# Kernel tuning notes

Measured on AMD Instinct MI355X. Metric: run time of the kernel, lower is better.

The kernel has to match this reference:

```python
import jax, jax.numpy as jnp
import numpy as np

SPATIAL_SHAPES = ((80, 80), (40, 40), (20, 20))  # strides 8/16/32 on 640x640
NUM_HEADS = 8
N_POINTS = 4
D_MODEL = 256
OFFSET_SCALE = 0.5
N_LEVELS = len(SPATIAL_SHAPES)
TOTAL_P = N_LEVELS * N_POINTS


def setup_inputs() -> dict:
    key = jax.random.key(0)
    ks = jax.random.split(key, 11)
    B, Q = 32, 300
    S = sum(h * w for h, w in SPATIAL_SHAPES)  # 8400
    d = D_MODEL
    s = 0.02
    return {
        "hidden_states": jax.random.normal(ks[0], (B, Q, d), jnp.float32),
        "encoder_hidden_states": jax.random.normal(ks[1], (B, S, d), jnp.float32),
        "reference_points": jax.random.uniform(ks[2], (B, Q, 1, 4), jnp.float32, 0.1, 0.9),
        "W_off": jax.random.normal(ks[3], (d, NUM_HEADS * TOTAL_P * 2), jnp.float32) * s,
        "b_off": jax.random.normal(ks[4], (NUM_HEADS * TOTAL_P * 2,), jnp.float32) * s,
        "W_attn": jax.random.normal(ks[5], (d, NUM_HEADS * TOTAL_P), jnp.float32) * s,
        "b_attn": jax.random.normal(ks[6], (NUM_HEADS * TOTAL_P,), jnp.float32) * s,
        "W_val": jax.random.normal(ks[7], (d, d), jnp.float32) * s,
        "b_val": jax.random.normal(ks[8], (d,), jnp.float32) * s,
        "W_out": jax.random.normal(ks[9], (d, d), jnp.float32) * s,
        "b_out": jax.random.normal(ks[10], (d,), jnp.float32) * s,
    }


def _bilinear_sample(img, grid):
    # img: (N, H, W, C); grid: (N, Q, P, 2), normalized coords in [-1, 1]
    # torch grid_sample(mode='bilinear', padding_mode='zeros', align_corners=False)
    N, Hh, Ww, C = img.shape
    gx = (grid[..., 0] + 1.0) * (Ww * 0.5) - 0.5
    gy = (grid[..., 1] + 1.0) * (Hh * 0.5) - 0.5
    x0 = jnp.floor(gx)
    y0 = jnp.floor(gy)
    wx1 = gx - x0
    wx0 = 1.0 - wx1
    wy1 = gy - y0
    wy0 = 1.0 - wy1
    n_idx = jnp.arange(N)[:, None, None]

    def tap(ix, iy, w):
        valid = (ix >= 0) & (ix < Ww) & (iy >= 0) & (iy < Hh)
        ixc = jnp.clip(ix, 0, Ww - 1).astype(jnp.int32)
        iyc = jnp.clip(iy, 0, Hh - 1).astype(jnp.int32)
        v = img[n_idx, iyc, ixc]  # (N, Q, P, C)
        return v * (w * valid.astype(w.dtype))[..., None]

    return (tap(x0, y0, wx0 * wy0) + tap(x0 + 1.0, y0, wx1 * wy0)
            + tap(x0, y0 + 1.0, wx0 * wy1) + tap(x0 + 1.0, y0 + 1.0, wx1 * wy1))


def reference(hidden_states, encoder_hidden_states, reference_points,
              W_off, b_off, W_attn, b_attn, W_val, b_val, W_out, b_out):
    B, Q, d = hidden_states.shape
    S = encoder_hidden_states.shape[1]
    H = NUM_HEADS
    C = d // H

    value = (encoder_hidden_states @ W_val + b_val).reshape(B, S, H, C)
    offs = (hidden_states @ W_off + b_off).reshape(B, Q, H, TOTAL_P, 2)
    attn = jax.nn.softmax((hidden_states @ W_attn + b_attn).reshape(B, Q, H, TOTAL_P), axis=-1)

    # 4-d reference points branch (boxes): loc = ref_xy + off * (1/P) * ref_wh * offset_scale
    n_points_scale = jnp.full((TOTAL_P, 1), 1.0 / N_POINTS, hidden_states.dtype)
    loc = (reference_points[:, :, None, :, :2]
           + offs * n_points_scale * reference_points[:, :, None, :, 2:] * OFFSET_SCALE)
    grids = 2.0 * loc - 1.0  # method='default'
    grids = grids.transpose(0, 2, 1, 3, 4).reshape(B * H, Q, TOTAL_P, 2)

    value_bh = value.transpose(0, 2, 1, 3).reshape(B * H, S, C)

    samples = []
    start = 0
    p0 = 0
    for (h, w) in SPATIAL_SHAPES:
        v_l = value_bh[:, start:start + h * w].reshape(B * H, h, w, C)
        g_l = grids[:, :, p0:p0 + N_POINTS]
        samples.append(_bilinear_sample(v_l, g_l))
        start += h * w
        p0 += N_POINTS
    sampled = jnp.concatenate(samples, axis=2)  # (B*H, Q, TOTAL_P, C)

    attn_bh = attn.transpose(0, 2, 1, 3).reshape(B * H, Q, TOTAL_P)
    out = jnp.einsum("nqpc,nqp->nqc", sampled, attn_bh)  # (B*H, Q, C)
    out = out.reshape(B, H, Q, C).transpose(0, 2, 1, 3).reshape(B, Q, H * C)
    return out @ W_out + b_out
```

## Files before the change

### kernel.cpp

```cpp
#include <hip/hip_runtime.h>
#include <hip/hip_fp16.h>

#define DEVI __device__ __forceinline__

typedef _Float16 f16x8 __attribute__((ext_vector_type(8)));
typedef float f32x4 __attribute__((ext_vector_type(4)));

static DEVI unsigned short f2h_u(float f) {
    _Float16 h = (_Float16)f;
    return __builtin_bit_cast(unsigned short, h);
}
static DEVI float h2f_u(unsigned short u) {
    return (float)__builtin_bit_cast(_Float16, u);
}
static DEVI unsigned pk2(float a, float b) {
    return (unsigned)f2h_u(a) | ((unsigned)f2h_u(b) << 16);
}


__global__ __launch_bounds__(256) void prep_weights(
    const float* __restrict__ W_val, const float* __restrict__ W_off,
    const float* __restrict__ W_attn, const float* __restrict__ W_out,
    const float* __restrict__ b_off, const float* __restrict__ b_attn,
    unsigned short* __restrict__ Wvt, unsigned short* __restrict__ Wct,
    unsigned short* __restrict__ Wot, float* __restrict__ cbias)
{
    int idx = blockIdx.x * 256 + threadIdx.x;
    if (idx < 65536) {
        int n = idx >> 8, k = idx & 255;
        Wvt[idx] = f2h_u(W_val[k * 256 + n]);
    } else if (idx < 65536 + 73728) {
        int j = idx - 65536;
        int n = j >> 8, k = j & 255;
        Wct[j] = f2h_u(n < 192 ? W_off[k * 192 + n] : W_attn[k * 96 + (n - 192)]);
    } else if (idx < 204800) {
        int j = idx - 139264;
        int n = j >> 8, k = j & 255;
        Wot[j] = f2h_u(W_out[k * 256 + n]);
    } else if (idx < 205088) {
        int j = idx - 204800;
        cbias[j] = (j < 192) ? b_off[j] : b_attn[j - 192];
    }
}

template<int BN, bool OUT_F16>
__global__ __launch_bounds__(256) void gemm_f16(
    const float* __restrict__ A, const unsigned short* __restrict__ Wt,
    const float* __restrict__ bias, void* __restrict__ outp, int ldo)
{
    constexpr int NI  = BN / 16;
    constexpr int LDA = 40;
    constexpr int LDB = 40;
    constexpr int LDC = BN + 4;
    constexpr int SM1 = 64 * LDA * 2 + BN * LDB * 2;
    constexpr int SM2 = 64 * LDC * 4;
    constexpr int SMEM = SM1 > SM2 ? SM1 : SM2;
    __shared__ __align__(16) char smem[SMEM];
    unsigned short* As = (unsigned short*)smem;
    unsigned short* Bs = (unsigned short*)(smem + 64 * LDA * 2);
    float* Cs = (float*)smem;

    const int tid  = threadIdx.x;
    const int wave = tid >> 6;
    const int lane = tid & 63;
    const int l15  = lane & 15;
    const int qd   = lane >> 4;
    const int m0   = blockIdx.y * 64;
    const int n0   = blockIdx.x * BN;

    f32x4 acc[NI];
#pragma unroll
    for (int i = 0; i < NI; i++) acc[i] = (f32x4){0.f, 0.f, 0.f, 0.f};

#pragma unroll
    for (int kt = 0; kt < 8; kt++) {
#pragma unroll
        for (int i = 0; i < 2; i++) {
            int f = tid + i * 256;
            int row = f >> 3, c4 = f & 7;
            const float4 v = *(const float4*)(A + (size_t)(m0 + row) * 256 + kt * 32 + c4 * 4);
            uint2 p;
            p.x = pk2(v.x, v.y);
            p.y = pk2(v.z, v.w);
            *(uint2*)&As[row * LDA + c4 * 4] = p;
        }
        for (int f = tid; f < BN * 4; f += 256) {
            int row = f >> 2, ch = f & 3;
            uint4 v = *(const uint4*)(Wt + (size_t)(n0 + row) * 256 + kt * 32 + ch * 8);
            *(uint4*)&Bs[row * LDB + ch * 8] = v;
        }
        __syncthreads();
        f16x8 af = *(const f16x8*)&As[(wave * 16 + l15) * LDA + qd * 8];
#pragma unroll
        for (int ni = 0; ni < NI; ni++) {
            f16x8 fb = *(const f16x8*)&Bs[(ni * 16 + l15) * LDB + qd * 8];
            acc[ni] = __builtin_amdgcn_mfma_f32_16x16x32_f16(af, fb, acc[ni], 0, 0, 0);
        }
        __syncthreads();
    }

#pragma unroll
    for (int ni = 0; ni < NI; ni++) {
#pragma unroll
        for (int r = 0; r < 4; r++) {
            Cs[(wave * 16 + qd * 4 + r) * LDC + ni * 16 + l15] = acc[ni][r];
        }
    }
    __syncthreads();
    for (int f = tid; f < 64 * (BN / 4); f += 256) {
        int row = f / (BN / 4), c4 = f % (BN / 4);
        float4 v = *(const float4*)&Cs[row * LDC + c4 * 4];
        const float4 bb = *(const float4*)(bias + n0 + c4 * 4);
        v.x += bb.x; v.y += bb.y; v.z += bb.z; v.w += bb.w;
        if (OUT_F16) {
            uint2 p;
            p.x = pk2(v.x, v.y);
            p.y = pk2(v.z, v.w);
            *(uint2*)((unsigned short*)outp + (size_t)(m0 + row) * ldo + n0 + c4 * 4) = p;
        } else {
            *(float4*)((float*)outp + (size_t)(m0 + row) * ldo + n0 + c4 * 4) = v;
        }
    }
}

__global__ __launch_bounds__(256) void sample_attn(
    const float* __restrict__ P, const float* __restrict__ refp,
    const unsigned short* __restrict__ val, float* __restrict__ out_attn)
{
    __shared__ float sLog[8][12];
    __shared__ float sLoc[8][12][3];
    const int row = blockIdx.x;
    const int b = row / 300;
    const int tid = threadIdx.x;

    const float4 r4 = *(const float4*)(refp + (size_t)row * 4);

    int h = 0, p = 0;
    float offx = 0.f, offy = 0.f, logit = 0.f;
    if (tid < 96) {
        h = tid / 12;
        p = tid - h * 12;
        const float* Pr = P + (size_t)row * 288;
        offx  = Pr[h * 24 + p * 2];
        offy  = Pr[h * 24 + p * 2 + 1];
        logit = Pr[192 + h * 12 + p];
        sLog[h][p] = logit;
    }
    __syncthreads();
    if (tid < 96) {
        float m = -1e30f;
#pragma unroll
        for (int j = 0; j < 12; j++) m = fmaxf(m, sLog[h][j]);
        float s = 0.f;
#pragma unroll
        for (int j = 0; j < 12; j++) s += expf(sLog[h][j] - m);
        float w = expf(logit - m) / s;
        sLoc[h][p][0] = r4.x + offx * 0.125f * r4.z;
        sLoc[h][p][1] = r4.y + offy * 0.125f * r4.w;
        sLoc[h][p][2] = w;
    }
    __syncthreads();

    const int hh = tid >> 5, c = tid & 31;
    const unsigned short* vb = val + (size_t)b * 8400 * 256 + hh * 32 + c;
    float acc = 0.f;
#pragma unroll
    for (int p2 = 0; p2 < 12; p2++) {
        const int lvl  = p2 >> 2;
        const int W    = (lvl == 0) ? 80 : ((lvl == 1) ? 40 : 20);
        const int Hh   = W;
        const int loff = (lvl == 0) ? 0 : ((lvl == 1) ? 6400 : 8000);
        const float lx = sLoc[hh][p2][0];
        const float ly = sLoc[hh][p2][1];
        const float w  = sLoc[hh][p2][2];
        const float px = lx * (float)W - 0.5f;
        const float py = ly * (float)Hh - 0.5f;
        const float x0f = floorf(px), y0f = floorf(py);
        const float fx = px - x0f, fy = py - y0f;
        const int x0 = (int)x0f, y0 = (int)y0f;
        const int x1 = x0 + 1, y1 = y0 + 1;
        const float w00 = (1.f - fx) * (1.f - fy);
        const float w10 = fx * (1.f - fy);
        const float w01 = (1.f - fx) * fy;
        const float w11 = fx * fy;
        const bool vx0 = (x0 >= 0) && (x0 < W);
        const bool vx1 = (x1 >= 0) && (x1 < W);
        const bool vy0 = (y0 >= 0) && (y0 < Hh);
        const bool vy1 = (y1 >= 0) && (y1 < Hh);
        const int x0c = min(max(x0, 0), W - 1), x1c = min(max(x1, 0), W - 1);
        const int y0c = min(max(y0, 0), Hh - 1), y1c = min(max(y1, 0), Hh - 1);
        const float v00 = h2f_u(vb[(size_t)(loff + y0c * W + x0c) * 256]);
        const float v10 = h2f_u(vb[(size_t)(loff + y0c * W + x1c) * 256]);
        const float v01 = h2f_u(vb[(size_t)(loff + y1c * W + x0c) * 256]);
        const float v11 = h2f_u(vb[(size_t)(loff + y1c * W + x1c) * 256]);
        float sv = 0.f;
        sv += (vx0 && vy0) ? w00 * v00 : 0.f;
        sv += (vx1 && vy0) ? w10 * v10 : 0.f;
        sv += (vx0 && vy1) ? w01 * v01 : 0.f;
        sv += (vx1 && vy1) ? w11 * v11 : 0.f;
        acc += w * sv;
    }
    out_attn[(size_t)row * 256 + tid] = acc;
}

extern "C" void kernel_launch(void* const* d_in, const int* in_sizes, int n_in,
                              void* d_out, int out_size, void* d_ws, size_t ws_size,
                              hipStream_t stream)
{
    const float* hs     = (const float*)d_in[0];
    const float* enc    = (const float*)d_in[1];
    const float* refp   = (const float*)d_in[2];
    const float* W_off  = (const float*)d_in[3];
    const float* b_off  = (const float*)d_in[4];
    const float* W_attn = (const float*)d_in[5];
    const float* b_attn = (const float*)d_in[6];
    const float* W_val  = (const float*)d_in[7];
    const float* b_val  = (const float*)d_in[8];
    const float* W_out  = (const float*)d_in[9];
    const float* b_out  = (const float*)d_in[10];
    float* outp = (float*)d_out;

    char* ws = (char*)d_ws;
    unsigned short* val = (unsigned short*)ws;
    float* P            = (float*)(ws + 137625600);
    float* oattn        = (float*)(ws + 148684800);
    unsigned short* Wvt = (unsigned short*)(ws + 158515200);
    unsigned short* Wct = (unsigned short*)(ws + 158646272);
    unsigned short* Wot = (unsigned short*)(ws + 158793728);
    float* cbias        = (float*)(ws + 158924800);

    prep_weights<<<802, 256, 0, stream>>>(W_val, W_off, W_attn, W_out,
                                          b_off, b_attn, Wvt, Wct, Wot, cbias);
    gemm_f16<144, false><<<dim3(2, 150), 256, 0, stream>>>(hs, Wct, cbias, P, 288);
    gemm_f16<128, true ><<<dim3(2, 4200), 256, 0, stream>>>(enc, Wvt, b_val, val, 256);
    sample_attn<<<9600, 256, 0, stream>>>(P, refp, val, oattn);
    gemm_f16<128, false><<<dim3(2, 150), 256, 0, stream>>>(oattn, Wot, b_out, outp, 256);
}
```

Measured before the change: 543.0 us.

## Prefetch GEMM tiles into registers and write f16 epilogue directly

The GEMM main loop now loads the next k-tile of A and W into registers while the current tile is being multiplied, so global loads overlap with MFMA work. The f16-output path adds the bias and converts to half before staging, which halves the shared-memory footprint and lets stores be 16-byte wide. The small projection GEMMs also use narrower N tiles (96 and 64) so they launch more blocks. The risks are higher register pressure from the prefetch buffers and more redundant A loads across the extra N blocks.

```diff
diff --git a/kernel.cpp b/kernel.cpp
--- a/kernel.cpp
+++ b/kernel.cpp
@@ -49,16 +49,18 @@
     const float* __restrict__ bias, void* __restrict__ outp, int ldo)
 {
     constexpr int NI  = BN / 16;
+    constexpr int NB  = (BN * 4 + 255) / 256;
+    constexpr bool BEXACT = (BN * 4 % 256) == 0;
     constexpr int LDA = 40;
     constexpr int LDB = 40;
     constexpr int LDC = BN + 4;
+    constexpr int LDH = BN + 8;
     constexpr int SM1 = 64 * LDA * 2 + BN * LDB * 2;
-    constexpr int SM2 = 64 * LDC * 4;
+    constexpr int SM2 = OUT_F16 ? (64 * LDH * 2) : (64 * LDC * 4);
     constexpr int SMEM = SM1 > SM2 ? SM1 : SM2;
     __shared__ __align__(16) char smem[SMEM];
     unsigned short* As = (unsigned short*)smem;
     unsigned short* Bs = (unsigned short*)(smem + 64 * LDA * 2);
-    float* Cs = (float*)smem;
 
     const int tid  = threadIdx.x;
     const int wave = tid >> 6;
@@ -68,56 +70,97 @@
     const int m0   = blockIdx.y * 64;
     const int n0   = blockIdx.x * BN;
 
+    const int ar0 = tid >> 3;
+    const int ac0 = (tid & 7) * 4;
+    const float* aptr0 = A + (size_t)(m0 + ar0) * 256 + ac0;
+    const float* aptr1 = aptr0 + 32 * 256;
+
     f32x4 acc[NI];
 #pragma unroll
     for (int i = 0; i < NI; i++) acc[i] = (f32x4){0.f, 0.f, 0.f, 0.f};
 
+    float4 apf0 = *(const float4*)(aptr0);
+    float4 apf1 = *(const float4*)(aptr1);
+    uint4 bpf[NB];
+#pragma unroll
+    for (int j = 0; j < NB; j++) {
+        int f = tid + j * 256;
+        if (BEXACT || f < BN * 4) {
+            int row = f >> 2, ch = f & 3;
+            bpf[j] = *(const uint4*)(Wt + (size_t)(n0 + row) * 256 + ch * 8);
+        }
+    }
+
 #pragma unroll
     for (int kt = 0; kt < 8; kt++) {
-#pragma unroll
-        for (int i = 0; i < 2; i++) {
-            int f = tid + i * 256;
-            int row = f >> 3, c4 = f & 7;
-            const float4 v = *(const float4*)(A + (size_t)(m0 + row) * 256 + kt * 32 + c4 * 4);
-            uint2 p;
-            p.x = pk2(v.x, v.y);
-            p.y = pk2(v.z, v.w);
-            *(uint2*)&As[row * LDA + c4 * 4] = p;
-        }
-        for (int f = tid; f < BN * 4; f += 256) {
-            int row = f >> 2, ch = f & 3;
-            uint4 v = *(const uint4*)(Wt + (size_t)(n0 + row) * 256 + kt * 32 + ch * 8);
-            *(uint4*)&Bs[row * LDB + ch * 8] = v;
+        if (kt) __syncthreads();
+        {
+            uint2 p0; p0.x = pk2(apf0.x, apf0.y); p0.y = pk2(apf0.z, apf0.w);
+            *(uint2*)&As[ar0 * LDA + ac0] = p0;
+            uint2 p1; p1.x = pk2(apf1.x, apf1.y); p1.y = pk2(apf1.z, apf1.w);
+            *(uint2*)&As[(ar0 + 32) * LDA + ac0] = p1;
+        }
+#pragma unroll
+        for (int j = 0; j < NB; j++) {
+            int f = tid + j * 256;
+            if (BEXACT || f < BN * 4) {
+                int row = f >> 2, ch = f & 3;
+                *(uint4*)&Bs[row * LDB + ch * 8] = bpf[j];
+            }
         }
         __syncthreads();
+        if (kt < 7) {
+            apf0 = *(const float4*)(aptr0 + (kt + 1) * 32);
+            apf1 = *(const float4*)(aptr1 + (kt + 1) * 32);
+#pragma unroll
+            for (int j = 0; j < NB; j++) {
+                int f = tid + j * 256;
+                if (BEXACT || f < BN * 4) {
+                    int row = f >> 2, ch = f & 3;
+                    bpf[j] = *(const uint4*)(Wt + (size_t)(n0 + row) * 256 + (kt + 1) * 32 + ch * 8);
+                }
+            }
+        }
         f16x8 af = *(const f16x8*)&As[(wave * 16 + l15) * LDA + qd * 8];
 #pragma unroll
         for (int ni = 0; ni < NI; ni++) {
             f16x8 fb = *(const f16x8*)&Bs[(ni * 16 + l15) * LDB + qd * 8];
             acc[ni] = __builtin_amdgcn_mfma_f32_16x16x32_f16(af, fb, acc[ni], 0, 0, 0);
         }
+    }
+    __syncthreads();
+
+    if (OUT_F16) {
+        unsigned short* Ch = (unsigned short*)smem;
+#pragma unroll
+        for (int ni = 0; ni < NI; ni++) {
+            const float bb = bias[n0 + ni * 16 + l15];
+#pragma unroll
+            for (int r = 0; r < 4; r++) {
+                Ch[(wave * 16 + qd * 4 + r) * LDH + ni * 16 + l15] = f2h_u(acc[ni][r] + bb);
+            }
+        }
         __syncthreads();
-    }
-
-#pragma unroll
-    for (int ni = 0; ni < NI; ni++) {
-#pragma unroll
-        for (int r = 0; r < 4; r++) {
-            Cs[(wave * 16 + qd * 4 + r) * LDC + ni * 16 + l15] = acc[ni][r];
-        }
-    }
-    __syncthreads();
-    for (int f = tid; f < 64 * (BN / 4); f += 256) {
-        int row = f / (BN / 4), c4 = f % (BN / 4);
-        float4 v = *(const float4*)&Cs[row * LDC + c4 * 4];
-        const float4 bb = *(const float4*)(bias + n0 + c4 * 4);
-        v.x += bb.x; v.y += bb.y; v.z += bb.z; v.w += bb.w;
-        if (OUT_F16) {
-            uint2 p;
-            p.x = pk2(v.x, v.y);
-            p.y = pk2(v.z, v.w);
-            *(uint2*)((unsigned short*)outp + (size_t)(m0 + row) * ldo + n0 + c4 * 4) = p;
-        } else {
+        for (int f = tid; f < 64 * (BN / 8); f += 256) {
+            int row = f / (BN / 8), c8 = f % (BN / 8);
+            uint4 v = *(uint4*)&Ch[row * LDH + c8 * 8];
+            *(uint4*)((unsigned short*)outp + (size_t)(m0 + row) * ldo + n0 + c8 * 8) = v;
+        }
+    } else {
+        float* Cs = (float*)smem;
+#pragma unroll
+        for (int ni = 0; ni < NI; ni++) {
+#pragma unroll
+            for (int r = 0; r < 4; r++) {
+                Cs[(wave * 16 + qd * 4 + r) * LDC + ni * 16 + l15] = acc[ni][r];
+            }
+        }
+        __syncthreads();
+        for (int f = tid; f < 64 * (BN / 4); f += 256) {
+            int row = f / (BN / 4), c4 = f % (BN / 4);
+            float4 v = *(const float4*)&Cs[row * LDC + c4 * 4];
+            const float4 bb = *(const float4*)(bias + n0 + c4 * 4);
+            v.x += bb.x; v.y += bb.y; v.z += bb.z; v.w += bb.w;
             *(float4*)((float*)outp + (size_t)(m0 + row) * ldo + n0 + c4 * 4) = v;
         }
     }
@@ -231,8 +274,8 @@
 
     prep_weights<<<802, 256, 0, stream>>>(W_val, W_off, W_attn, W_out,
                                           b_off, b_attn, Wvt, Wct, Wot, cbias);
-    gemm_f16<144, false><<<dim3(2, 150), 256, 0, stream>>>(hs, Wct, cbias, P, 288);
+    gemm_f16<96, false><<<dim3(3, 150), 256, 0, stream>>>(hs, Wct, cbias, P, 288);
     gemm_f16<128, true ><<<dim3(2, 4200), 256, 0, stream>>>(enc, Wvt, b_val, val, 256);
     sample_attn<<<9600, 256, 0, stream>>>(P, refp, val, oattn);
-    gemm_f16<128, false><<<dim3(2, 150), 256, 0, stream>>>(oattn, Wot, b_out, outp, 256);
-}
+    gemm_f16<64, false><<<dim3(4, 150), 256, 0, stream>>>(oattn, Wot, b_out, outp, 256);
+}
```

Result: slower. 628.4 us (+15.7%).
